# Optimization experiments

Hardware: AMD Instinct MI355X
Metric: run time of the kernel (lower is better)

The kernel has to match this reference:

```python
import jax, jax.numpy as jnp
import numpy as np

N = 768          # n_nuclei
EMB = 32         # embedding_dim
RBF = 32         # rbf_dim
CUTOFF = 10.0    # rbf_cutoff
MAXQ = 10        # max(charges)


def _edges(n):
    # fully-connected edge list exactly as in GNN.__call__
    senders = np.arange(n).repeat(n - 1)
    recv = np.arange(n)[None].repeat(n - 1, axis=0)
    recv = (recv + np.arange(n - 1)[:, None] + 1) % n
    return jnp.asarray(senders), jnp.asarray(recv.reshape(-1))


def _mlp2(x, w0, b0, w1, b1=None):
    # AutoMLP(out_dim, depth=2): Dense+silu, Dense (final_bias optional)
    h = jax.nn.silu(x @ w0 + b0)
    y = h @ w1
    return y if b1 is None else y + b1


def _seg_mean(vals, seg, n):
    s = jax.ops.segment_sum(vals, seg, num_segments=n, indices_are_sorted=True)
    c = jax.ops.segment_sum(jnp.ones((vals.shape[0], 1), vals.dtype), seg,
                            num_segments=n, indices_are_sorted=True)
    return s / jnp.maximum(c, 1.0)


def setup_inputs() -> dict:
    key = jax.random.key(0)
    ki = iter(jax.random.split(key, 48))

    def W(din, dout):
        return jax.random.normal(next(ki), (din, dout), jnp.float32) / np.sqrt(din).astype(np.float32)

    def b(d):
        return jax.random.normal(next(ki), (d,), jnp.float32) * 0.01

    return dict(
        nuclei=jax.random.normal(next(ki), (N, 3), jnp.float32) * 3.0,
        charges=jax.random.randint(next(ki), (N,), 0, MAXQ),
        f=(jnp.arange(RBF, dtype=jnp.float32) + 1.0) * jnp.pi,  # BesselRBF param init
        embed_table=jax.random.normal(next(ki), (MAXQ, EMB), jnp.float32),
        mp1_w0=W(96, 32), mp1_b0=b(32), mp1_w1=W(32, 32), mp1_b1=b(32),
        up1_w0=W(64, 64), up1_b0=b(64), up1_w1=W(64, 64), up1_b1=b(64),
        mp2_w0=W(160, 32), mp2_b0=b(32), mp2_w1=W(32, 32), mp2_b1=b(32),
        up2_w0=W(96, 64), up2_b0=b(64), up2_w1=W(64, 64), up2_b1=b(64),
        no_w0=W(160, 3), no_b0=b(3), no_w1=W(3, 3),
        no_embed=jax.random.normal(next(ki), (MAXQ, 3), jnp.float32) * 0.1,
        go_w0=W(160, 1), go_b0=b(1), go_w1=W(1, 1), go_b1=b(1),
    )


def reference(nuclei, charges, f, embed_table,
              mp1_w0, mp1_b0, mp1_w1, mp1_b1,
              up1_w0, up1_b0, up1_w1, up1_b1,
              mp2_w0, mp2_b0, mp2_w1, mp2_b1,
              up2_w0, up2_b0, up2_w1, up2_b1,
              no_w0, no_b0, no_w1, no_embed,
              go_w0, go_b0, go_w1, go_b1):
    nuclei = nuclei.reshape(-1, 3) @ jnp.eye(3, dtype=nuclei.dtype)  # constants 'axes'
    n = nuclei.shape[0]
    senders, receivers = _edges(n)

    # BesselRBF on pairwise distances
    d = jnp.linalg.norm(nuclei[senders] - nuclei[receivers], axis=-1)
    x_ext = d[:, None] + 1e-8
    e_embed = jnp.sqrt(2.0 / CUTOFF) * jnp.sin(f * x_ext / CUTOFF) / x_ext  # [E, RBF]

    n_embed = embed_table[charges]  # [N, EMB]
    embeddings = [n_embed]

    # layer 1: msg out 32, update out 64 (no residual: 32 != 64)
    edge_in = jnp.concatenate([n_embed[senders], n_embed[receivers], e_embed], axis=-1)
    msg = _seg_mean(_mlp2(edge_in, mp1_w0, mp1_b0, mp1_w1, mp1_b1), senders, n)
    upd = _mlp2(jnp.concatenate([n_embed, msg], axis=-1), up1_w0, up1_b0, up1_w1, up1_b1)
    n_embed = upd  # dims differ -> plain replacement
    embeddings.append(n_embed)

    # layer 2: msg out 32, update out 64 (residual: 64 == 64)
    edge_in = jnp.concatenate([n_embed[senders], n_embed[receivers], e_embed], axis=-1)
    msg = _seg_mean(_mlp2(edge_in, mp2_w0, mp2_b0, mp2_w1, mp2_b1), senders, n)
    upd = _mlp2(jnp.concatenate([n_embed, msg], axis=-1), up2_w0, up2_b0, up2_w1, up2_b1)
    n_embed = n_embed + upd
    embeddings.append(n_embed)

    agg = jnp.concatenate(embeddings, axis=-1)  # [N, 32+64+64=160]

    node_out = _mlp2(agg, no_w0, no_b0, no_w1) + no_embed[charges]  # [N, 3]
    global_out = _mlp2(jnp.mean(agg, axis=0), go_w0, go_b0, go_w1, go_b1)  # [1]
    return (node_out, global_out)
```

## Files before the change

kernel.cpp:

```cpp
#include <hip/hip_runtime.h>
#include <hip/hip_bf16.h>

typedef __hip_bfloat16 bf16;
typedef __attribute__((ext_vector_type(8))) short short8;
typedef __attribute__((ext_vector_type(4))) float float4v;

#define NN   768
#define NEPS 767

#define C_NUC   0
#define C_F     2304
#define C_MP1W0 2656
#define C_MP1B0 5728
#define C_MP1W1 5760
#define C_MP1B1 6784
#define C_UP1W0 6816
#define C_UP1B0 10912
#define C_UP1W1 10976
#define C_UP1B1 15072
#define C_MP2W0 15136
#define C_MP2B0 20256
#define C_MP2W1 20288
#define C_MP2B1 21312
#define C_UP2W0 21344
#define C_UP2B0 27488
#define C_UP2W1 27552
#define C_UP2B1 31648
#define C_NOW0  31712
#define C_NOB0  32192
#define C_NOW1  32195
#define C_NOEMB 32204
#define C_GOW0  32234
#define C_GOB0  32394
#define C_GOW1  32395
#define C_GOB1  32396
__device__ __align__(16) float g_c[32400];

#define OFF_EMB0 0
#define OFF_SA1  24576
#define OFF_SB1  49152
#define OFF_EMB1 73728
#define OFF_SA2  122880
#define OFF_SB2  147456
__device__ float g_ws[172032];
__device__ float g_agg[640];
__device__ int   g_cnt;
__device__ int   g_isf;
__device__ short8 g_rbf[NN*48*64];

struct Ptrs { const void* p[28]; };

__device__ __forceinline__ float b2f(bf16 v){ return __bfloat162float(v); }
__device__ __forceinline__ float LD(const void* p, int i, int f32){
  return f32 ? ((const float*)p)[i] : b2f(((const bf16*)p)[i]);
}
__device__ __forceinline__ int detect_f32(const void* f){
  float v = ((const float*)f)[0];
  return (fabsf(v - 3.14159265f) < 0.01f) ? 1 : 0;
}
__device__ __forceinline__ float fast_rcp(float x){ return __builtin_amdgcn_rcpf(x); }
__device__ __forceinline__ float silu_f(float p){ return p * fast_rcp(1.f + __expf(-p)); }
__device__ __forceinline__ unsigned short rne_bf16(float x){
  unsigned int b = __float_as_uint(x);
  return (unsigned short)((b + 0x7fffu + ((b >> 16) & 1u)) >> 16);
}
__device__ __forceinline__ void cv(const void* p, int off, int sz, int gt, int isf){
  for (int i = gt; i < sz; i += 96*256) g_c[off + i] = LD(p, i, isf);
}

__launch_bounds__(256)
__global__ void k_conv_prep(Ptrs P, const int* __restrict__ charges){
  int t = threadIdx.x;
  int gt = blockIdx.x*256 + t;
  int isf = detect_f32(P.p[2]);
  if (gt == 0){ g_isf = isf; g_cnt = 0; }
  if (gt < 640) g_agg[gt] = 0.f;

  cv(P.p[0],  C_NUC,   2304, gt, isf);
  cv(P.p[2],  C_F,     32,   gt, isf);
  cv(P.p[4],  C_MP1W0, 3072, gt, isf);
  cv(P.p[5],  C_MP1B0, 32,   gt, isf);
  cv(P.p[6],  C_MP1W1, 1024, gt, isf);
  cv(P.p[7],  C_MP1B1, 32,   gt, isf);
  cv(P.p[8],  C_UP1W0, 4096, gt, isf);
  cv(P.p[9],  C_UP1B0, 64,   gt, isf);
  cv(P.p[10], C_UP1W1, 4096, gt, isf);
  cv(P.p[11], C_UP1B1, 64,   gt, isf);
  cv(P.p[12], C_MP2W0, 5120, gt, isf);
  cv(P.p[13], C_MP2B0, 32,   gt, isf);
  cv(P.p[14], C_MP2W1, 1024, gt, isf);
  cv(P.p[15], C_MP2B1, 32,   gt, isf);
  cv(P.p[16], C_UP2W0, 6144, gt, isf);
  cv(P.p[17], C_UP2B0, 64,   gt, isf);
  cv(P.p[18], C_UP2W1, 4096, gt, isf);
  cv(P.p[19], C_UP2B1, 64,   gt, isf);
  cv(P.p[20], C_NOW0,  480,  gt, isf);
  cv(P.p[21], C_NOB0,  3,    gt, isf);
  cv(P.p[22], C_NOW1,  9,    gt, isf);
  cv(P.p[23], C_NOEMB, 30,   gt, isf);
  cv(P.p[24], C_GOW0,  160,  gt, isf);
  cv(P.p[25], C_GOB0,  1,    gt, isf);
  cv(P.p[26], C_GOW1,  1,    gt, isf);
  cv(P.p[27], C_GOB1,  1,    gt, isf);

  __shared__ float w0L[2048];
  __shared__ float rowL[8][32];
  for (int idx = t; idx < 2048; idx += 256) w0L[idx] = LD(P.p[4], idx, isf);
  int nd = t >> 5, col = t & 31;
  int node = blockIdx.x*8 + nd;
  int ch = charges[node];
  float v = LD(P.p[3], ch*32 + col, isf);
  g_ws[OFF_EMB0 + node*32 + col] = v;
  rowL[nd][col] = v;
  __syncthreads();
  float sa = 0.f, sb = 0.f;
  #pragma unroll
  for (int k = 0; k < 32; k++){
    float rv = rowL[nd][k];
    sa = fmaf(rv, w0L[k*32 + col],      sa);
    sb = fmaf(rv, w0L[(32+k)*32 + col], sb);
  }
  g_ws[OFF_SA1 + node*32 + col] = sa;
  g_ws[OFF_SB1 + node*32 + col] = sb;
}

__launch_bounds__(256)
__global__ void k_edge1(){
  __shared__ __align__(16) float pos[NN*3];
  __shared__ __align__(16) float w1L[1024];
  __shared__ float wsum[4][32];
  __shared__ float hsumL[32];
  __shared__ float msgL[32];
  __shared__ float catU[64], hU[64], e1U[64], part[256];

  int i = blockIdx.x, t = threadIdx.x;
  int w = t >> 6, lane = t & 63, q = lane >> 4, c = lane & 15;

  {
    const float4* src = (const float4*)(g_c + C_NUC);
    float4* dst = (float4*)pos;
    for (int idx = t; idx < 576; idx += 256) dst[idx] = src[idx];
    ((float4*)w1L)[t] = ((const float4*)(g_c + C_MP1W1))[t];
  }
  const float* SA = g_ws + OFF_SA1;
  const float* SB = g_ws + OFF_SB1;
  short8 bfr0, bfr1;
  #pragma unroll
  for (int j = 0; j < 8; j++){
    int row = q*8 + j;
    bfr0[j] = (short)rne_bf16(g_c[C_MP1W0 + 2048 + row*32 + c]);
    bfr1[j] = (short)rne_bf16(g_c[C_MP1W0 + 2048 + row*32 + 16 + c]);
  }
  float preB0 = SA[i*32 + c]      + g_c[C_MP1B0 + c];
  float preB1 = SA[i*32 + 16 + c] + g_c[C_MP1B0 + 16 + c];
  float fj[8];
  #pragma unroll
  for (int j = 0; j < 8; j++) fj[j] = g_c[C_F + q*8 + j] * 0.1f;
  __syncthreads();

  float px = pos[i*3], py = pos[i*3+1], pz = pos[i*3+2];

  float xs[12], scv[12];
  #pragma unroll
  for (int s = 0; s < 12; s++){
    int el = (w + s*4)*16 + c;
    int ela = (el < NEPS) ? el : 0;
    int r = ela + (ela >= i);
    float dx = px - pos[r*3], dy = py - pos[r*3+1], dz = pz - pos[r*3+2];
    float d = sqrtf(fmaf(dx, dx, fmaf(dy, dy, dz*dz)));
    xs[s] = d + 1e-8f;
    scv[s] = 0.44721359549995793f * fast_rcp(xs[s]);
  }

  float sum0 = 0.f, sum1 = 0.f;
  #pragma unroll 4
  for (int s = 0; s < 12; s++){
    int tl = w + s*4;
    float sb0[4], sb1[4];
    #pragma unroll
    for (int p = 0; p < 4; p++){
      int el2 = tl*16 + q*4 + p;
      int e2a = (el2 < NEPS) ? el2 : 0;
      int r2 = e2a + (e2a >= i);
      sb0[p] = SB[r2*32 + c];
      sb1[p] = SB[r2*32 + 16 + c];
    }
    short8 af;
    #pragma unroll
    for (int j = 0; j < 8; j++) af[j] = (short)rne_bf16(scv[s] * __sinf(fj[j]*xs[s]));
    g_rbf[(i*48 + tl)*64 + lane] = af;
    float4v z = {0.f, 0.f, 0.f, 0.f};
    float4v a0 = __builtin_amdgcn_mfma_f32_16x16x32_bf16(af, bfr0, z, 0, 0, 0);
    float4v a1 = __builtin_amdgcn_mfma_f32_16x16x32_bf16(af, bfr1, z, 0, 0, 0);
    #pragma unroll
    for (int p = 0; p < 4; p++){
      int el2 = tl*16 + q*4 + p;
      if (el2 < NEPS){
        sum0 += silu_f(a0[p] + preB0 + sb0[p]);
        sum1 += silu_f(a1[p] + preB1 + sb1[p]);
      }
    }
  }
  sum0 += __shfl_xor(sum0, 16); sum0 += __shfl_xor(sum0, 32);
  sum1 += __shfl_xor(sum1, 16); sum1 += __shfl_xor(sum1, 32);
  if (lane < 16){ wsum[w][lane] = sum0; wsum[w][16 + lane] = sum1; }
  __syncthreads();
  if (t < 32) hsumL[t] = wsum[0][t] + wsum[1][t] + wsum[2][t] + wsum[3][t];
  __syncthreads();
  if (t < 32){
    float y = 0.f;
    #pragma unroll
    for (int m = 0; m < 32; m++) y = fmaf(hsumL[m], w1L[m*32 + t], y);
    msgL[t] = y * (1.f/767.f) + g_c[C_MP1B1 + t];
  }

  if (t < 32){
    catU[t] = g_ws[OFF_EMB0 + i*32 + t];
    catU[32 + t] = msgL[t];
  }
  __syncthreads();

  int g = t >> 6, col = t & 63;
  {
    const float* w0 = g_c + C_UP1W0;
    float p0 = 0.f;
    #pragma unroll
    for (int j = 0; j < 16; j++){ int k = g*16 + j; p0 = fmaf(catU[k], w0[k*64 + col], p0); }
    part[t] = p0;
  }
  __syncthreads();
  if (t < 64) hU[t] = silu_f(g_c[C_UP1B0 + t] + part[t] + part[64+t] + part[128+t] + part[192+t]);
  __syncthreads();
  {
    const float* w1u = g_c + C_UP1W1;
    float p1 = 0.f;
    #pragma unroll
    for (int j = 0; j < 16; j++){ int k = g*16 + j; p1 = fmaf(hU[k], w1u[k*64 + col], p1); }
    part[t] = p1;
  }
  __syncthreads();
  if (t < 64){
    float y = g_c[C_UP1B1 + t] + part[t] + part[64+t] + part[128+t] + part[192+t];
    e1U[t] = y;
    g_ws[OFF_EMB1 + i*64 + t] = y;
  }
  __syncthreads();
  {
    int half = t >> 7, g2 = (t >> 5) & 3, c32 = t & 31;
    const float* m2 = g_c + C_MP2W0;
    float p2 = 0.f;
    #pragma unroll
    for (int j = 0; j < 16; j++){
      int k = g2*16 + j;
      p2 = fmaf(e1U[k], m2[(half*64 + k)*32 + c32], p2);
    }
    part[t] = p2;
  }
  __syncthreads();
  if (t < 64){
    int half = t >> 5, c32 = t & 31;
    float s = part[half*128 + c32] + part[half*128 + 32 + c32]
            + part[half*128 + 64 + c32] + part[half*128 + 96 + c32];
    if (half == 0) g_ws[OFF_SA2 + i*32 + c32] = s;
    else           g_ws[OFF_SB2 + i*32 + c32] = s;
  }
}

__launch_bounds__(256)
__global__ void k_edge2(const int* __restrict__ charges, void* __restrict__ out){
  __shared__ __align__(16) float w1L[1024];
  __shared__ float wsum[4][32];
  __shared__ float hsumL[32];
  __shared__ float msgL[32];
  __shared__ float catU[96], hU[64], aggL[160], noL[522], h3L[3], part[256];
  __shared__ int lastL;

  int i = blockIdx.x, t = threadIdx.x;
  int w = t >> 6, lane = t & 63, q = lane >> 4, c = lane & 15;

  ((float4*)w1L)[t] = ((const float4*)(g_c + C_MP2W1))[t];
  const float* SA = g_ws + OFF_SA2;
  const float* SB = g_ws + OFF_SB2;
  short8 bfr0, bfr1;
  #pragma unroll
  for (int j = 0; j < 8; j++){
    int row = q*8 + j;
    bfr0[j] = (short)rne_bf16(g_c[C_MP2W0 + 4096 + row*32 + c]);
    bfr1[j] = (short)rne_bf16(g_c[C_MP2W0 + 4096 + row*32 + 16 + c]);
  }
  float preB0 = SA[i*32 + c]      + g_c[C_MP2B0 + c];
  float preB1 = SA[i*32 + 16 + c] + g_c[C_MP2B0 + 16 + c];

  float sum0 = 0.f, sum1 = 0.f;
  short8 afA = g_rbf[(i*48 + w)*64 + lane];
  float sbA0[4], sbA1[4];
  #pragma unroll
  for (int p = 0; p < 4; p++){
    int el2 = w*16 + q*4 + p;
    int e2a = (el2 < NEPS) ? el2 : 0;
    int r2 = e2a + (e2a >= i);
    sbA0[p] = SB[r2*32 + c];
    sbA1[p] = SB[r2*32 + 16 + c];
  }
  #pragma unroll
  for (int s = 0; s < 12; s++){
    int tl = w + s*4;
    short8 afB;
    float sbB0[4], sbB1[4];
    if (s < 11){
      int tn = tl + 4;
      afB = g_rbf[(i*48 + tn)*64 + lane];
      #pragma unroll
      for (int p = 0; p < 4; p++){
        int el2 = tn*16 + q*4 + p;
        int e2a = (el2 < NEPS) ? el2 : 0;
        int r2 = e2a + (e2a >= i);
        sbB0[p] = SB[r2*32 + c];
        sbB1[p] = SB[r2*32 + 16 + c];
      }
    }
    float4v z = {0.f, 0.f, 0.f, 0.f};
    float4v a0 = __builtin_amdgcn_mfma_f32_16x16x32_bf16(afA, bfr0, z, 0, 0, 0);
    float4v a1 = __builtin_amdgcn_mfma_f32_16x16x32_bf16(afA, bfr1, z, 0, 0, 0);
    #pragma unroll
    for (int p = 0; p < 4; p++){
      int el2 = tl*16 + q*4 + p;
      if (el2 < NEPS){
        sum0 += silu_f(a0[p] + preB0 + sbA0[p]);
        sum1 += silu_f(a1[p] + preB1 + sbA1[p]);
      }
    }
    if (s < 11){
      afA = afB;
      #pragma unroll
      for (int p = 0; p < 4; p++){ sbA0[p] = sbB0[p]; sbA1[p] = sbB1[p]; }
    }
  }
  sum0 += __shfl_xor(sum0, 16); sum0 += __shfl_xor(sum0, 32);
  sum1 += __shfl_xor(sum1, 16); sum1 += __shfl_xor(sum1, 32);
  if (lane < 16){ wsum[w][lane] = sum0; wsum[w][16 + lane] = sum1; }
  __syncthreads();
  if (t < 32) hsumL[t] = wsum[0][t] + wsum[1][t] + wsum[2][t] + wsum[3][t];
  __syncthreads();
  if (t < 32){
    float y = 0.f;
    #pragma unroll
    for (int m = 0; m < 32; m++) y = fmaf(hsumL[m], w1L[m*32 + t], y);
    msgL[t] = y * (1.f/767.f) + g_c[C_MP2B1 + t];
  }

  if (t < 64) catU[t] = g_ws[OFF_EMB1 + i*64 + t];
  if (t < 32){ catU[64 + t] = msgL[t]; aggL[t] = g_ws[OFF_EMB0 + i*32 + t]; }
  for (int idx = t; idx < 522; idx += 256) noL[idx] = g_c[C_NOW0 + idx];
  __syncthreads();

  int g = t >> 6, col = t & 63;
  {
    const float* w0 = g_c + C_UP2W0;
    float p0 = 0.f;
    #pragma unroll
    for (int j = 0; j < 24; j++){ int k = g*24 + j; p0 = fmaf(catU[k], w0[k*64 + col], p0); }
    part[t] = p0;
  }
  __syncthreads();
  if (t < 64) hU[t] = silu_f(g_c[C_UP2B0 + t] + part[t] + part[64+t] + part[128+t] + part[192+t]);
  __syncthreads();
  {
    const float* w1u = g_c + C_UP2W1;
    float p1 = 0.f;
    #pragma unroll
    for (int j = 0; j < 16; j++){ int k = g*16 + j; p1 = fmaf(hU[k], w1u[k*64 + col], p1); }
    part[t] = p1;
  }
  __syncthreads();
  if (t < 64){
    float y = g_c[C_UP2B1 + t] + part[t] + part[64+t] + part[128+t] + part[192+t];
    float e2 = catU[t] + y;
    aggL[32 + t] = catU[t];
    aggL[96 + t] = e2;
  }
  __syncthreads();
  if (t < 48){
    int chunk = t / 3, c3 = t - chunk*3;
    float p = 0.f;
    #pragma unroll
    for (int j = 0; j < 10; j++){ int k = chunk*10 + j; p = fmaf(aggL[k], noL[k*3 + c3], p); }
    part[t] = p;
  }
  __syncthreads();
  if (t < 3){
    float p = noL[480 + t];
    #pragma unroll
    for (int ch = 0; ch < 16; ch++) p += part[ch*3 + t];
    h3L[t] = silu_f(p);
  }
  __syncthreads();
  if (t < 3){
    float o = 0.f;
    #pragma unroll
    for (int m = 0; m < 3; m++) o = fmaf(h3L[m], noL[483 + m*3 + t], o);
    o += noL[492 + charges[i]*3 + t];
    if (g_isf) ((float*)out)[i*3 + t] = o;
    else       ((bf16*)out)[i*3 + t] = __float2bfloat16(o);
  }
  if (t < 160) atomicAdd(&g_agg[(i & 3)*160 + t], aggL[t]);
  __syncthreads();
  if (t == 0) lastL = (atomicAdd(&g_cnt, 1) == NN - 1) ? 1 : 0;
  __syncthreads();
  if (lastL){
    float v = 0.f;
    if (t < 160){
      float s = atomicAdd(&g_agg[t], 0.f) + atomicAdd(&g_agg[160 + t], 0.f)
              + atomicAdd(&g_agg[320 + t], 0.f) + atomicAdd(&g_agg[480 + t], 0.f);
      v = s * (1.f/768.f) * g_c[C_GOW0 + t];
    }
    part[t] = v;
    __syncthreads();
    if (t == 0){
      float tot = 0.f;
      for (int k = 0; k < 160; k++) tot += part[k];
      float h = silu_f(tot + g_c[C_GOB0]);
      float go = h * g_c[C_GOW1] + g_c[C_GOB1];
      if (g_isf) ((float*)out)[2304] = go;
      else       ((bf16*)out)[2304] = __float2bfloat16(go);
    }
  }
}

extern "C" void kernel_launch(void* const* d_in, const int* in_sizes, int n_in,
                              void* d_out, int out_size, void* d_ws, size_t ws_size,
                              hipStream_t stream) {
  Ptrs P;
  for (int k = 0; k < 28; k++) P.p[k] = d_in[k];
  const int* charges = (const int*)d_in[1];

  k_conv_prep<<<96, 256, 0, stream>>>(P, charges);
  k_edge1<<<NN, 256, 0, stream>>>();
  k_edge2<<<NN, 256, 0, stream>>>(charges, d_out);
}
```

Baseline: 169.2 us.

## Recompute RBF features in second edge kernel and double block size to 512

The second edge kernel now recomputes the Bessel RBF features from positions instead of reading a large bf16 buffer that the first kernel used to write, so that global buffer goes away. Both edge kernels run 512 threads per node (8 waves, 6 tiles each), and the small node MLP reductions are repartitioned to match. Packed bf16 conversion uses the v_cvt_pk_bf16_f32 instruction instead of manual rounding. In exchange the sin evaluations are done twice and the block needs more shared memory and synchronisation.

```diff
diff --git a/kernel.cpp b/kernel.cpp
--- a/kernel.cpp
+++ b/kernel.cpp
@@ -46,7 +46,6 @@
 __device__ float g_agg[640];
 __device__ int   g_cnt;
 __device__ int   g_isf;
-__device__ short8 g_rbf[NN*48*64];
 
 struct Ptrs { const void* p[28]; };
 
@@ -63,6 +62,11 @@
 __device__ __forceinline__ unsigned short rne_bf16(float x){
   unsigned int b = __float_as_uint(x);
   return (unsigned short)((b + 0x7fffu + ((b >> 16) & 1u)) >> 16);
+}
+__device__ __forceinline__ unsigned int cvtpk_bf16(float lo, float hi){
+  unsigned int r;
+  asm("v_cvt_pk_bf16_f32 %0, %1, %2" : "=v"(r) : "v"(lo), "v"(hi));
+  return r;
 }
 __device__ __forceinline__ void cv(const void* p, int off, int sz, int gt, int isf){
   for (int i = gt; i < sz; i += 96*256) g_c[off + i] = LD(p, i, isf);
@@ -124,14 +128,15 @@
   g_ws[OFF_SB1 + node*32 + col] = sb;
 }
 
-__launch_bounds__(256)
+__launch_bounds__(512)
 __global__ void k_edge1(){
   __shared__ __align__(16) float pos[NN*3];
   __shared__ __align__(16) float w1L[1024];
-  __shared__ float wsum[4][32];
+  __shared__ float wsum[8][32];
   __shared__ float hsumL[32];
   __shared__ float msgL[32];
-  __shared__ float catU[64], hU[64], e1U[64], part[256];
+  __shared__ float catU[64], hU[64], e1U[64];
+  __shared__ float part[512];
 
   int i = blockIdx.x, t = threadIdx.x;
   int w = t >> 6, lane = t & 63, q = lane >> 4, c = lane & 15;
@@ -139,8 +144,8 @@
   {
     const float4* src = (const float4*)(g_c + C_NUC);
     float4* dst = (float4*)pos;
-    for (int idx = t; idx < 576; idx += 256) dst[idx] = src[idx];
-    ((float4*)w1L)[t] = ((const float4*)(g_c + C_MP1W1))[t];
+    for (int idx = t; idx < 576; idx += 512) dst[idx] = src[idx];
+    if (t < 256) ((float4*)w1L)[t] = ((const float4*)(g_c + C_MP1W1))[t];
   }
   const float* SA = g_ws + OFF_SA1;
   const float* SB = g_ws + OFF_SB1;
@@ -160,10 +165,10 @@
 
   float px = pos[i*3], py = pos[i*3+1], pz = pos[i*3+2];
 
-  float xs[12], scv[12];
-  #pragma unroll
-  for (int s = 0; s < 12; s++){
-    int el = (w + s*4)*16 + c;
+  float xs[6], scv[6];
+  #pragma unroll
+  for (int s = 0; s < 6; s++){
+    int el = (w + s*8)*16 + c;
     int ela = (el < NEPS) ? el : 0;
     int r = ela + (ela >= i);
     float dx = px - pos[r*3], dy = py - pos[r*3+1], dz = pz - pos[r*3+2];
@@ -173,9 +178,9 @@
   }
 
   float sum0 = 0.f, sum1 = 0.f;
-  #pragma unroll 4
-  for (int s = 0; s < 12; s++){
-    int tl = w + s*4;
+  #pragma unroll
+  for (int s = 0; s < 6; s++){
+    int tl = w + s*8;
     float sb0[4], sb1[4];
     #pragma unroll
     for (int p = 0; p < 4; p++){
@@ -185,10 +190,13 @@
       sb0[p] = SB[r2*32 + c];
       sb1[p] = SB[r2*32 + 16 + c];
     }
-    short8 af;
-    #pragma unroll
-    for (int j = 0; j < 8; j++) af[j] = (short)rne_bf16(scv[s] * __sinf(fj[j]*xs[s]));
-    g_rbf[(i*48 + tl)*64 + lane] = af;
+    float sv[8];
+    #pragma unroll
+    for (int j = 0; j < 8; j++) sv[j] = scv[s] * __sinf(fj[j]*xs[s]);
+    union { short8 s8; unsigned int u[4]; } afu;
+    #pragma unroll
+    for (int h = 0; h < 4; h++) afu.u[h] = cvtpk_bf16(sv[2*h], sv[2*h+1]);
+    short8 af = afu.s8;
     float4v z = {0.f, 0.f, 0.f, 0.f};
     float4v a0 = __builtin_amdgcn_mfma_f32_16x16x32_bf16(af, bfr0, z, 0, 0, 0);
     float4v a1 = __builtin_amdgcn_mfma_f32_16x16x32_bf16(af, bfr1, z, 0, 0, 0);
@@ -205,7 +213,8 @@
   sum1 += __shfl_xor(sum1, 16); sum1 += __shfl_xor(sum1, 32);
   if (lane < 16){ wsum[w][lane] = sum0; wsum[w][16 + lane] = sum1; }
   __syncthreads();
-  if (t < 32) hsumL[t] = wsum[0][t] + wsum[1][t] + wsum[2][t] + wsum[3][t];
+  if (t < 32) hsumL[t] = wsum[0][t] + wsum[1][t] + wsum[2][t] + wsum[3][t]
+                       + wsum[4][t] + wsum[5][t] + wsum[6][t] + wsum[7][t];
   __syncthreads();
   if (t < 32){
     float y = 0.f;
@@ -225,60 +234,72 @@
     const float* w0 = g_c + C_UP1W0;
     float p0 = 0.f;
     #pragma unroll
-    for (int j = 0; j < 16; j++){ int k = g*16 + j; p0 = fmaf(catU[k], w0[k*64 + col], p0); }
+    for (int j = 0; j < 8; j++){ int k = g*8 + j; p0 = fmaf(catU[k], w0[k*64 + col], p0); }
     part[t] = p0;
   }
   __syncthreads();
-  if (t < 64) hU[t] = silu_f(g_c[C_UP1B0 + t] + part[t] + part[64+t] + part[128+t] + part[192+t]);
+  if (t < 64){
+    float s = part[t] + part[64+t] + part[128+t] + part[192+t]
+            + part[256+t] + part[320+t] + part[384+t] + part[448+t];
+    hU[t] = silu_f(g_c[C_UP1B0 + t] + s);
+  }
   __syncthreads();
   {
     const float* w1u = g_c + C_UP1W1;
     float p1 = 0.f;
     #pragma unroll
-    for (int j = 0; j < 16; j++){ int k = g*16 + j; p1 = fmaf(hU[k], w1u[k*64 + col], p1); }
+    for (int j = 0; j < 8; j++){ int k = g*8 + j; p1 = fmaf(hU[k], w1u[k*64 + col], p1); }
     part[t] = p1;
   }
   __syncthreads();
   if (t < 64){
-    float y = g_c[C_UP1B1 + t] + part[t] + part[64+t] + part[128+t] + part[192+t];
+    float s = part[t] + part[64+t] + part[128+t] + part[192+t]
+            + part[256+t] + part[320+t] + part[384+t] + part[448+t];
+    float y = g_c[C_UP1B1 + t] + s;
     e1U[t] = y;
     g_ws[OFF_EMB1 + i*64 + t] = y;
   }
   __syncthreads();
   {
-    int half = t >> 7, g2 = (t >> 5) & 3, c32 = t & 31;
+    int oc = t & 63;
     const float* m2 = g_c + C_MP2W0;
     float p2 = 0.f;
     #pragma unroll
-    for (int j = 0; j < 16; j++){
-      int k = g2*16 + j;
-      p2 = fmaf(e1U[k], m2[(half*64 + k)*32 + c32], p2);
+    for (int j = 0; j < 8; j++){
+      int k = g*8 + j;
+      p2 = fmaf(e1U[k], m2[((oc >> 5)*64 + k)*32 + (oc & 31)], p2);
     }
     part[t] = p2;
   }
   __syncthreads();
   if (t < 64){
-    int half = t >> 5, c32 = t & 31;
-    float s = part[half*128 + c32] + part[half*128 + 32 + c32]
-            + part[half*128 + 64 + c32] + part[half*128 + 96 + c32];
-    if (half == 0) g_ws[OFF_SA2 + i*32 + c32] = s;
-    else           g_ws[OFF_SB2 + i*32 + c32] = s;
-  }
-}
-
-__launch_bounds__(256)
+    float s = part[t] + part[64+t] + part[128+t] + part[192+t]
+            + part[256+t] + part[320+t] + part[384+t] + part[448+t];
+    if ((t >> 5) == 0) g_ws[OFF_SA2 + i*32 + (t & 31)] = s;
+    else               g_ws[OFF_SB2 + i*32 + (t & 31)] = s;
+  }
+}
+
+__launch_bounds__(512)
 __global__ void k_edge2(const int* __restrict__ charges, void* __restrict__ out){
+  __shared__ __align__(16) float pos[NN*3];
   __shared__ __align__(16) float w1L[1024];
-  __shared__ float wsum[4][32];
+  __shared__ float wsum[8][32];
   __shared__ float hsumL[32];
   __shared__ float msgL[32];
-  __shared__ float catU[96], hU[64], aggL[160], noL[522], h3L[3], part[256];
+  __shared__ float catU[96], hU[64], aggL[160], noL[522], h3L[3];
+  __shared__ float part[512];
   __shared__ int lastL;
 
   int i = blockIdx.x, t = threadIdx.x;
   int w = t >> 6, lane = t & 63, q = lane >> 4, c = lane & 15;
 
-  ((float4*)w1L)[t] = ((const float4*)(g_c + C_MP2W1))[t];
+  {
+    const float4* src = (const float4*)(g_c + C_NUC);
+    float4* dst = (float4*)pos;
+    for (int idx = t; idx < 576; idx += 512) dst[idx] = src[idx];
+    if (t < 256) ((float4*)w1L)[t] = ((const float4*)(g_c + C_MP2W1))[t];
+  }
   const float* SA = g_ws + OFF_SA2;
   const float* SB = g_ws + OFF_SB2;
   short8 bfr0, bfr1;
@@ -290,57 +311,63 @@
   }
   float preB0 = SA[i*32 + c]      + g_c[C_MP2B0 + c];
   float preB1 = SA[i*32 + 16 + c] + g_c[C_MP2B0 + 16 + c];
+  float fj[8];
+  #pragma unroll
+  for (int j = 0; j < 8; j++) fj[j] = g_c[C_F + q*8 + j] * 0.1f;
+  __syncthreads();
+
+  float px = pos[i*3], py = pos[i*3+1], pz = pos[i*3+2];
+
+  float xs[6], scv[6];
+  #pragma unroll
+  for (int s = 0; s < 6; s++){
+    int el = (w + s*8)*16 + c;
+    int ela = (el < NEPS) ? el : 0;
+    int r = ela + (ela >= i);
+    float dx = px - pos[r*3], dy = py - pos[r*3+1], dz = pz - pos[r*3+2];
+    float d = sqrtf(fmaf(dx, dx, fmaf(dy, dy, dz*dz)));
+    xs[s] = d + 1e-8f;
+    scv[s] = 0.44721359549995793f * fast_rcp(xs[s]);
+  }
 
   float sum0 = 0.f, sum1 = 0.f;
-  short8 afA = g_rbf[(i*48 + w)*64 + lane];
-  float sbA0[4], sbA1[4];
-  #pragma unroll
-  for (int p = 0; p < 4; p++){
-    int el2 = w*16 + q*4 + p;
-    int e2a = (el2 < NEPS) ? el2 : 0;
-    int r2 = e2a + (e2a >= i);
-    sbA0[p] = SB[r2*32 + c];
-    sbA1[p] = SB[r2*32 + 16 + c];
-  }
-  #pragma unroll
-  for (int s = 0; s < 12; s++){
-    int tl = w + s*4;
-    short8 afB;
-    float sbB0[4], sbB1[4];
-    if (s < 11){
-      int tn = tl + 4;
-      afB = g_rbf[(i*48 + tn)*64 + lane];
-      #pragma unroll
-      for (int p = 0; p < 4; p++){
-        int el2 = tn*16 + q*4 + p;
-        int e2a = (el2 < NEPS) ? el2 : 0;
-        int r2 = e2a + (e2a >= i);
-        sbB0[p] = SB[r2*32 + c];
-        sbB1[p] = SB[r2*32 + 16 + c];
-      }
-    }
+  #pragma unroll
+  for (int s = 0; s < 6; s++){
+    int tl = w + s*8;
+    float sb0[4], sb1[4];
+    #pragma unroll
+    for (int p = 0; p < 4; p++){
+      int el2 = tl*16 + q*4 + p;
+      int e2a = (el2 < NEPS) ? el2 : 0;
+      int r2 = e2a + (e2a >= i);
+      sb0[p] = SB[r2*32 + c];
+      sb1[p] = SB[r2*32 + 16 + c];
+    }
+    float sv[8];
+    #pragma unroll
+    for (int j = 0; j < 8; j++) sv[j] = scv[s] * __sinf(fj[j]*xs[s]);
+    union { short8 s8; unsigned int u[4]; } afu;
+    #pragma unroll
+    for (int h = 0; h < 4; h++) afu.u[h] = cvtpk_bf16(sv[2*h], sv[2*h+1]);
+    short8 af = afu.s8;
     float4v z = {0.f, 0.f, 0.f, 0.f};
-    float4v a0 = __builtin_amdgcn_mfma_f32_16x16x32_bf16(afA, bfr0, z, 0, 0, 0);
-    float4v a1 = __builtin_amdgcn_mfma_f32_16x16x32_bf16(afA, bfr1, z, 0, 0, 0);
+    float4v a0 = __builtin_amdgcn_mfma_f32_16x16x32_bf16(af, bfr0, z, 0, 0, 0);
+    float4v a1 = __builtin_amdgcn_mfma_f32_16x16x32_bf16(af, bfr1, z, 0, 0, 0);
     #pragma unroll
     for (int p = 0; p < 4; p++){
       int el2 = tl*16 + q*4 + p;
       if (el2 < NEPS){
-        sum0 += silu_f(a0[p] + preB0 + sbA0[p]);
-        sum1 += silu_f(a1[p] + preB1 + sbA1[p]);
+        sum0 += silu_f(a0[p] + preB0 + sb0[p]);
+        sum1 += silu_f(a1[p] + preB1 + sb1[p]);
       }
-    }
-    if (s < 11){
-      afA = afB;
-      #pragma unroll
-      for (int p = 0; p < 4; p++){ sbA0[p] = sbB0[p]; sbA1[p] = sbB1[p]; }
     }
   }
   sum0 += __shfl_xor(sum0, 16); sum0 += __shfl_xor(sum0, 32);
   sum1 += __shfl_xor(sum1, 16); sum1 += __shfl_xor(sum1, 32);
   if (lane < 16){ wsum[w][lane] = sum0; wsum[w][16 + lane] = sum1; }
   __syncthreads();
-  if (t < 32) hsumL[t] = wsum[0][t] + wsum[1][t] + wsum[2][t] + wsum[3][t];
+  if (t < 32) hsumL[t] = wsum[0][t] + wsum[1][t] + wsum[2][t] + wsum[3][t]
+                       + wsum[4][t] + wsum[5][t] + wsum[6][t] + wsum[7][t];
   __syncthreads();
   if (t < 32){
     float y = 0.f;
@@ -351,7 +378,7 @@
 
   if (t < 64) catU[t] = g_ws[OFF_EMB1 + i*64 + t];
   if (t < 32){ catU[64 + t] = msgL[t]; aggL[t] = g_ws[OFF_EMB0 + i*32 + t]; }
-  for (int idx = t; idx < 522; idx += 256) noL[idx] = g_c[C_NOW0 + idx];
+  for (int idx = t; idx < 522; idx += 512) noL[idx] = g_c[C_NOW0 + idx];
   __syncthreads();
 
   int g = t >> 6, col = t & 63;
@@ -359,22 +386,28 @@
     const float* w0 = g_c + C_UP2W0;
     float p0 = 0.f;
     #pragma unroll
-    for (int j = 0; j < 24; j++){ int k = g*24 + j; p0 = fmaf(catU[k], w0[k*64 + col], p0); }
+    for (int j = 0; j < 12; j++){ int k = g*12 + j; p0 = fmaf(catU[k], w0[k*64 + col], p0); }
     part[t] = p0;
   }
   __syncthreads();
-  if (t < 64) hU[t] = silu_f(g_c[C_UP2B0 + t] + part[t] + part[64+t] + part[128+t] + part[192+t]);
+  if (t < 64){
+    float s = part[t] + part[64+t] + part[128+t] + part[192+t]
+            + part[256+t] + part[320+t] + part[384+t] + part[448+t];
+    hU[t] = silu_f(g_c[C_UP2B0 + t] + s);
+  }
   __syncthreads();
   {
     const float* w1u = g_c + C_UP2W1;
     float p1 = 0.f;
     #pragma unroll
-    for (int j = 0; j < 16; j++){ int k = g*16 + j; p1 = fmaf(hU[k], w1u[k*64 + col], p1); }
+    for (int j = 0; j < 8; j++){ int k = g*8 + j; p1 = fmaf(hU[k], w1u[k*64 + col], p1); }
     part[t] = p1;
   }
   __syncthreads();
   if (t < 64){
-    float y = g_c[C_UP2B1 + t] + part[t] + part[64+t] + part[128+t] + part[192+t];
+    float s = part[t] + part[64+t] + part[128+t] + part[192+t]
+            + part[256+t] + part[320+t] + part[384+t] + part[448+t];
+    float y = g_c[C_UP2B1 + t] + s;
     float e2 = catU[t] + y;
     aggL[32 + t] = catU[t];
     aggL[96 + t] = e2;
@@ -435,6 +468,6 @@
   const int* charges = (const int*)d_in[1];
 
   k_conv_prep<<<96, 256, 0, stream>>>(P, charges);
-  k_edge1<<<NN, 256, 0, stream>>>();
-  k_edge2<<<NN, 256, 0, stream>>>(charges, d_out);
-}
+  k_edge1<<<NN, 512, 0, stream>>>();
+  k_edge2<<<NN, 512, 0, stream>>>(charges, d_out);
+}
```

Result: faster. 159.8 us (-5.5%).
